# Kernel optimization log

Hardware: AMD Instinct MI355X
Metric: run time of the kernel (lower is better)

The kernel has to match this reference:

```python
import jax, jax.numpy as jnp
import numpy as np

B, L, D = 2, 4096, 2048
H, K = 32, 16              # num_heads, mini_batch_size
HD = D // H                # head_dim = 64
NMB = L // K               # 256 mini-batches
TTT_BASE_LR = 1.0
LN_EPS = 1e-6


def setup_inputs() -> dict:
    key = jax.random.key(0)
    ks = jax.random.split(key, 16)
    r = lambda k, s: 0.02 * jax.random.normal(k, s, dtype=jnp.float32)
    return {
        "hidden_states": jax.random.normal(ks[0], (B, L, D), dtype=jnp.float32),
        "wq_w": r(ks[1], (D, D)), "wq_b": r(ks[2], (D,)),
        "wk_w": r(ks[3], (D, D)), "wk_b": r(ks[4], (D,)),
        "wv_w": r(ks[5], (D, D)), "wv_b": r(ks[6], (D,)),
        "wo_w": r(ks[7], (D, D)), "wo_b": r(ks[8], (D,)),
        "ttt_norm_weight": 1.0 + r(ks[9], (H, HD)),
        "ttt_norm_bias": r(ks[10], (H, HD)),
        "lr_w": r(ks[11], (H, 1, D)),       # learnable_ttt_lr_weight
        "lr_b": r(ks[12], (H, 1)),          # learnable_ttt_lr_bias
        "W1": r(ks[13], (H, HD, HD)),
        "b1": r(ks[14], (H, 1, HD)),
        "post_norm_w": jnp.ones((D,), jnp.float32),
        "post_norm_b": jnp.zeros((D,), jnp.float32),
    }


def ln_fwd(x, gamma, beta, eps=LN_EPS):
    mu = x.mean(-1, keepdims=True)
    var = ((x - mu) ** 2).mean(-1, keepdims=True)
    return gamma * ((x - mu) / jnp.sqrt(var + eps)) + beta


def ln_fused_l2_bwd(x, l2_target, gamma, beta, eps=LN_EPS):
    # grad of 0.5*||LN(x)*gamma+beta - target||^2 w.r.t. x (standard TTT helper)
    Dd = x.shape[-1]
    mu = x.mean(-1, keepdims=True)
    var = ((x - mu) ** 2).mean(-1, keepdims=True)
    std = jnp.sqrt(var + eps)
    x_hat = (x - mu) / std
    grad_x_hat = (gamma * x_hat + beta - l2_target) * gamma
    return (Dd * grad_x_hat
            - grad_x_hat.sum(-1, keepdims=True)
            - x_hat * (x_hat * grad_x_hat).sum(-1, keepdims=True)) / (Dd * std)


def reference(hidden_states, wq_w, wq_b, wk_w, wk_b, wv_w, wv_b, wo_w, wo_b,
              ttt_norm_weight, ttt_norm_bias, lr_w, lr_b, W1, b1,
              post_norm_w, post_norm_b):
    # QKV projections
    XQ = (hidden_states @ wq_w + wq_b).reshape(B, L, H, HD)
    XK = (hidden_states @ wk_w + wk_b).reshape(B, L, H, HD)
    XV = (hidden_states @ wv_w + wv_b).reshape(B, L, H, HD)
    # L2 normalize q/k per head (F.normalize, eps=1e-12)
    XQ = XQ / jnp.maximum(jnp.linalg.norm(XQ, axis=-1, keepdims=True), 1e-12)
    XK = XK / jnp.maximum(jnp.linalg.norm(XK, axis=-1, keepdims=True), 1e-12)
    # ln_reconstruction_target: torch.std is unbiased (ddof=1), eps added to std
    diff = XV - XK
    mu = diff.mean(-1, keepdims=True)
    std = jnp.std(diff, axis=-1, ddof=1, keepdims=True)
    XV = (ttt_norm_weight[None, None] * ((diff - mu) / (std + 1e-8))
          + ttt_norm_bias[None, None]) + XK
    # reshape to mini-batches: [B,H,NMB,K,HD]
    Xmb = hidden_states.reshape(B, NMB, K, D)
    tohd = lambda t: t.transpose(0, 2, 1, 3).reshape(B, H, NMB, K, HD)
    XQ, XK, XV = tohd(XQ), tohd(XK), tohd(XV)
    # eta gate: einsum('bnkc,hdc->bhnkd') with d==1, sigmoid, scale
    ttt_lr = jnp.einsum('bnkc,hdc->bhnkd', Xmb, lr_w) + lr_b.reshape(1, H, 1, 1, 1)
    ttt_lr = jax.nn.sigmoid(ttt_lr).transpose(0, 1, 2, 4, 3) * (TTT_BASE_LR / HD)  # [B,H,NMB,1,K]
    eta = jnp.broadcast_to(ttt_lr / K, (B, H, NMB, K, K))
    ln_w = ttt_norm_weight[:, None, :]  # [H,1,HD]
    ln_b = ttt_norm_bias[:, None, :]
    tril = jnp.tril(jnp.ones((K, K), jnp.float32))
    W1s = jnp.broadcast_to(W1[None], (B, H, HD, HD))
    b1s = jnp.broadcast_to(b1[None], (B, H, 1, HD))

    def step(carry, xs):
        W1c, b1c = carry
        xq, xk, xv, eta_mb = xs  # [B,H,K,HD], eta [B,H,K,K]
        Z1 = xk @ W1c + b1c
        grad = ln_fused_l2_bwd(Z1, xv - xk, ln_w, ln_b)        # [B,H,K,HD]
        Attn1 = tril * (xq @ xk.transpose(0, 1, 3, 2))         # causal within mini-batch
        b1_bar = b1c - (tril * eta_mb) @ grad
        Z1_bar = xq @ W1c - (eta_mb * Attn1) @ grad + b1_bar
        last_eta = eta_mb[:, :, -1, :, None]                   # [B,H,K,1]
        W1n = W1c - (last_eta * xk).transpose(0, 1, 3, 2) @ grad
        b1n = b1c - jnp.sum(last_eta * grad, axis=-2, keepdims=True)
        out = xq + ln_fwd(Z1_bar, ln_w, ln_b)
        return (W1n, b1n), out

    xs = tuple(t.transpose(2, 0, 1, 3, 4) for t in (XQ, XK, XV, eta))
    _, outs = jax.lax.scan(step, (W1s, b1s), xs)               # [NMB,B,H,K,HD]
    y = outs.transpose(1, 0, 3, 2, 4).reshape(B, L, D)
    # post_norm LayerNorm(eps=1e-6) then output projection
    mu = y.mean(-1, keepdims=True)
    var = ((y - mu) ** 2).mean(-1, keepdims=True)
    y = (y - mu) / jnp.sqrt(var + 1e-6) * post_norm_w + post_norm_b
    return y @ wo_w + wo_b
```

## Files before the change

kernel.cpp:

```cpp
#include <hip/hip_runtime.h>
#include <hip/hip_bf16.h>
#include <cstdint>
#include <cstddef>

#define DEV __device__ __forceinline__

constexpr int Bb = 2, Ls = 4096, Dd = 2048, Hh = 32, HD = 64, MBK = 16, NMBc = 256;
constexpr int MTOK = Bb * Ls;

typedef __bf16 bf16x8 __attribute__((ext_vector_type(8)));
typedef float  f32x4  __attribute__((ext_vector_type(4)));

DEV unsigned short f2bf(float f) {
    union { float f; unsigned int u; } x; x.f = f;
    unsigned int u = x.u;
    return (unsigned short)((u + 0x7fffu + ((u >> 16) & 1u)) >> 16);
}
DEV float b2f(unsigned short u) {
    union { unsigned int i; float f; } x; x.i = ((unsigned int)u) << 16;
    return x.f;
}

DEV float wsum64(float v) {
    int t;
    t = __builtin_amdgcn_update_dpp(0, __float_as_int(v), 0x111, 0xf, 0xf, true); v += __int_as_float(t);
    t = __builtin_amdgcn_update_dpp(0, __float_as_int(v), 0x112, 0xf, 0xf, true); v += __int_as_float(t);
    t = __builtin_amdgcn_update_dpp(0, __float_as_int(v), 0x114, 0xf, 0xf, true); v += __int_as_float(t);
    t = __builtin_amdgcn_update_dpp(0, __float_as_int(v), 0x118, 0xf, 0xf, true); v += __int_as_float(t);
    t = __builtin_amdgcn_update_dpp(0, __float_as_int(v), 0x142, 0xa, 0xf, true); v += __int_as_float(t);
    t = __builtin_amdgcn_update_dpp(0, __float_as_int(v), 0x143, 0xc, 0xf, true); v += __int_as_float(t);
    return __int_as_float(__builtin_amdgcn_readlane(__float_as_int(v), 63));
}

DEV void g2l16(const void* g, void* l) {
    __builtin_amdgcn_global_load_lds(
        (__attribute__((address_space(1))) void*)(g),
        (__attribute__((address_space(3))) void*)(l), 16, 0, 0);
}

__global__ __launch_bounds__(256) void cast_hs_kernel(const float* __restrict__ src,
                                                      unsigned short* __restrict__ dst) {
    int i = (blockIdx.x * 256 + threadIdx.x) * 4;
    float4 v = *(const float4*)(src + i);
    ushort4 o; o.x = f2bf(v.x); o.y = f2bf(v.y); o.z = f2bf(v.z); o.w = f2bf(v.w);
    *(ushort4*)(dst + i) = o;
}

__global__ __launch_bounds__(256) void transpose_cast_kernel(const float* __restrict__ W,
                                                             unsigned short* __restrict__ Wt) {
    __shared__ float tile[64][65];
    int bx = blockIdx.x & 31;
    int by = blockIdx.x >> 5;
    int t = threadIdx.x;
    int r = t >> 4, c4 = (t & 15) * 4;
    #pragma unroll
    for (int i = 0; i < 4; ++i) {
        int row = r + i * 16;
        float4 v = *(const float4*)(W + (size_t)(bx * 64 + row) * Dd + by * 64 + c4);
        tile[row][c4 + 0] = v.x; tile[row][c4 + 1] = v.y;
        tile[row][c4 + 2] = v.z; tile[row][c4 + 3] = v.w;
    }
    __syncthreads();
    #pragma unroll
    for (int i = 0; i < 4; ++i) {
        int row = r + i * 16;
        ushort4 o;
        o.x = f2bf(tile[c4 + 0][row]); o.y = f2bf(tile[c4 + 1][row]);
        o.z = f2bf(tile[c4 + 2][row]); o.w = f2bf(tile[c4 + 3][row]);
        *(ushort4*)(Wt + (size_t)(by * 64 + row) * Dd + bx * 64 + c4) = o;
    }
}

__global__ __launch_bounds__(256) void gemm_bt_kernel(const unsigned short* __restrict__ A,
                                                      const unsigned short* __restrict__ Bt,
                                                      const float* __restrict__ bias,
                                                      float* __restrict__ C,
                                                      int M, int N, int Kd) {
    __shared__ unsigned short sA[128 * 64];
    __shared__ unsigned short sB[128 * 64];
    int t = threadIdx.x;
    int lane = t & 63;
    int wid = t >> 6, wm = wid >> 1, wn = wid & 1;
    int quad = lane >> 4, c = lane & 15;
    int bm = blockIdx.x, bn = blockIdx.y;

    const unsigned short* pa[4]; const unsigned short* pb[4];
    unsigned short* la[4]; unsigned short* lb[4];
    #pragma unroll
    for (int i = 0; i < 4; ++i) {
        int lin = i * 256 + t;
        int row = lin >> 3, blk = lin & 7;
        int oct = blk ^ (row & 7);
        pa[i] = A  + (size_t)(bm * 128 + row) * Kd + oct * 8;
        pb[i] = Bt + (size_t)(bn * 128 + row) * Kd + oct * 8;
        la[i] = sA + lin * 8;
        lb[i] = sB + lin * 8;
    }

    f32x4 acc[4][4];
    #pragma unroll
    for (int i = 0; i < 4; ++i)
        #pragma unroll
        for (int j = 0; j < 4; ++j)
            #pragma unroll
            for (int r = 0; r < 4; ++r) acc[i][j][r] = 0.f;

    const char* sAc = (const char*)sA;
    const char* sBc = (const char*)sB;
    int rowA0 = wm * 64 + c, rowB0 = wn * 64 + c;
    int sw = (c & 7);

    int nkt = Kd >> 6;
    for (int kt = 0; kt < nkt; ++kt) {
        #pragma unroll
        for (int i = 0; i < 4; ++i) {
            g2l16(pa[i], la[i]);
            g2l16(pb[i], lb[i]);
            pa[i] += 64; pb[i] += 64;
        }
        __syncthreads();
        #pragma unroll
        for (int s = 0; s < 2; ++s) {
            bf16x8 af[4], bfv[4];
            int so = (s << 2) | quad;
            #pragma unroll
            for (int mt = 0; mt < 4; ++mt)
                af[mt] = *(const bf16x8*)(sAc + (rowA0 + mt * 16) * 128 + ((so ^ sw) * 16));
            #pragma unroll
            for (int nt = 0; nt < 4; ++nt)
                bfv[nt] = *(const bf16x8*)(sBc + (rowB0 + nt * 16) * 128 + ((so ^ sw) * 16));
            #pragma unroll
            for (int mt = 0; mt < 4; ++mt)
                #pragma unroll
                for (int nt = 0; nt < 4; ++nt)
                    acc[mt][nt] = __builtin_amdgcn_mfma_f32_16x16x32_bf16(af[mt], bfv[nt], acc[mt][nt], 0, 0, 0);
        }
        __syncthreads();
    }

    float bv[4];
    #pragma unroll
    for (int nt = 0; nt < 4; ++nt) bv[nt] = bias[bn * 128 + wn * 64 + nt * 16 + c];
    #pragma unroll
    for (int mt = 0; mt < 4; ++mt)
        #pragma unroll
        for (int r = 0; r < 4; ++r) {
            int row = bm * 128 + wm * 64 + mt * 16 + quad * 4 + r;
            float* cp = C + (size_t)row * N + bn * 128 + wn * 64 + c;
            #pragma unroll
            for (int nt = 0; nt < 4; ++nt) cp[nt * 16] = acc[mt][nt][r] + bv[nt];
        }
}

__global__ __launch_bounds__(256) void fixup_kernel(float* __restrict__ XQ, float* __restrict__ XK,
                                                    float* __restrict__ XV,
                                                    const float* __restrict__ lnw_g,
                                                    const float* __restrict__ lnb_g) {
    int g = blockIdx.x * 4 + (threadIdx.x >> 6);
    int d = threadIdx.x & 63;
    int h = g & (Hh - 1);
    size_t base = (size_t)(g >> 5) * Dd + h * 64 + d;
    float q = XQ[base], k = XK[base], v = XV[base];
    float nq = sqrtf(wsum64(q * q)); q /= fmaxf(nq, 1e-12f);
    float nk = sqrtf(wsum64(k * k)); k /= fmaxf(nk, 1e-12f);
    float diff = v - k;
    float mu = wsum64(diff) * (1.f / 64.f);
    float cc = diff - mu;
    float var = wsum64(cc * cc) * (1.f / 63.f);
    float vn = lnw_g[h * 64 + d] * cc / (sqrtf(var) + 1e-8f) + lnb_g[h * 64 + d] + k;
    XQ[base] = q; XK[base] = k; XV[base] = vn;
}

__global__ __launch_bounds__(256) void lr_kernel(const float* __restrict__ hs,
                                                 const float* __restrict__ lrw,
                                                 const float* __restrict__ lrb,
                                                 float* __restrict__ lr_out) {
    int tok = blockIdx.x;
    int t = threadIdx.x;
    int h = t >> 3, j0 = t & 7;
    const float* row = hs + (size_t)tok * Dd;
    const float* wr = lrw + (size_t)h * Dd;
    float p = 0.f;
    for (int j = j0 * 4; j < Dd; j += 32) {
        float4 a = *(const float4*)(row + j);
        float4 w = *(const float4*)(wr + j);
        p += a.x * w.x + a.y * w.y + a.z * w.z + a.w * w.w;
    }
    __shared__ float red[32][8];
    red[h][j0] = p;
    __syncthreads();
    if (t < 32) {
        float s = 0.f;
        #pragma unroll
        for (int i = 0; i < 8; ++i) s += red[t][i];
        s += lrb[t];
        s = 1.f / (1.f + expf(-s));
        s *= 1.0f / (HD * MBK);
        int b = tok >> 12, l = tok & (Ls - 1);
        lr_out[(size_t)(b * Hh + t) * Ls + l] = s;
    }
}

__global__ __launch_bounds__(256, 1) void scan_kernel(const float* __restrict__ XQ,
                                                      const float* __restrict__ XK,
                                                      const float* __restrict__ XV,
                                                      const float* __restrict__ lrbuf,
                                                      const float* __restrict__ W1in,
                                                      const float* __restrict__ b1in,
                                                      const float* __restrict__ lnw_g,
                                                      const float* __restrict__ lnb_g,
                                                      float* __restrict__ Y) {
    int bh = blockIdx.x;
    int b = bh >> 5, h = bh & 31;
    int t = threadIdx.x;
    int w = t >> 6;
    int lane = t & 63;
    int q = lane >> 4, n = lane & 15;
    int gc = 16 * w + n;

    __shared__ float tiles[2][3][16 * 68];
    __shared__ float svb[2][16];
    __shared__ unsigned short wt_hi[64 * 72];
    __shared__ unsigned short wt_lo[64 * 72];
    __shared__ float zT[64 * 20];
    __shared__ float zbT[64 * 20];
    __shared__ unsigned short gbufT[64 * 32];
    __shared__ unsigned short sxkT[64 * 32];
    __shared__ float att32[16 * 32];
    __shared__ float pb[4 * 64];

    #pragma unroll
    for (int i = 0; i < 16; ++i) {
        int k = i * 4 + w;
        float val = W1in[(size_t)h * 4096 + (size_t)k * 64 + lane];
        unsigned short hi = f2bf(val);
        unsigned short lo = f2bf(val - b2f(hi));
        wt_hi[lane * 72 + k] = hi;
        wt_lo[lane * 72 + k] = lo;
    }
    #pragma unroll
    for (int i = 0; i < 8; ++i) { gbufT[i * 256 + t] = 0; sxkT[i * 256 + t] = 0; }
    #pragma unroll
    for (int i = 0; i < 2; ++i) att32[i * 256 + t] = 0.f;

    float b1r = b1in[h * 64 + lane];
    float lnwr = lnw_g[h * 64 + lane];
    float lnbr = lnb_g[h * 64 + lane];

    const size_t gbase = ((size_t)b * Ls) * Dd + h * 64;
    const float* lrp = lrbuf + (size_t)bh * Ls;

    int rowp = t >> 4, c4p = (t & 15) * 4;
    *(float4*)&tiles[0][0][rowp * 68 + c4p] = *(const float4*)(XQ + gbase + (size_t)rowp * Dd + c4p);
    *(float4*)&tiles[0][1][rowp * 68 + c4p] = *(const float4*)(XK + gbase + (size_t)rowp * Dd + c4p);
    *(float4*)&tiles[0][2][rowp * 68 + c4p] = *(const float4*)(XV + gbase + (size_t)rowp * Dd + c4p);
    if (t < 16) svb[0][t] = lrp[t];
    float4 preq = *(const float4*)(XQ + gbase + (size_t)(16 + rowp) * Dd + c4p);
    float4 prek = *(const float4*)(XK + gbase + (size_t)(16 + rowp) * Dd + c4p);
    float4 prev = *(const float4*)(XV + gbase + (size_t)(16 + rowp) * Dd + c4p);
    float presv = (t < 16) ? lrp[16 + t] : 0.f;
    __syncthreads();

    const f32x4 zero4 = {0.f, 0.f, 0.f, 0.f};

    for (int nmb = 0; nmb < NMBc; ++nmb) {
        int cb = nmb & 1, nb2 = cb ^ 1;
        int l0 = nmb * 16;
        *(float4*)&tiles[nb2][0][rowp * 68 + c4p] = preq;
        *(float4*)&tiles[nb2][1][rowp * 68 + c4p] = prek;
        *(float4*)&tiles[nb2][2][rowp * 68 + c4p] = prev;
        if (t < 16) svb[nb2][t] = presv;
        int lp = (l0 + 32 <= Ls - 16) ? (l0 + 32) : (Ls - 16);
        preq = *(const float4*)(XQ + gbase + (size_t)(lp + rowp) * Dd + c4p);
        prek = *(const float4*)(XK + gbase + (size_t)(lp + rowp) * Dd + c4p);
        prev = *(const float4*)(XV + gbase + (size_t)(lp + rowp) * Dd + c4p);
        presv = (t < 16) ? lrp[lp + t] : 0.f;

        const float* xqs = &tiles[cb][0][0];
        const float* xks = &tiles[cb][1][0];
        const float* xvs = &tiles[cb][2][0];

        bf16x8 qf0, qf1, kf0, kf1;
        {
            float4 a0 = *(const float4*)&xqs[n * 68 + 8 * q];
            float4 a1 = *(const float4*)&xqs[n * 68 + 8 * q + 4];
            float4 a2 = *(const float4*)&xqs[n * 68 + 32 + 8 * q];
            float4 a3 = *(const float4*)&xqs[n * 68 + 32 + 8 * q + 4];
            qf0[0]=(__bf16)a0.x; qf0[1]=(__bf16)a0.y; qf0[2]=(__bf16)a0.z; qf0[3]=(__bf16)a0.w;
            qf0[4]=(__bf16)a1.x; qf0[5]=(__bf16)a1.y; qf0[6]=(__bf16)a1.z; qf0[7]=(__bf16)a1.w;
            qf1[0]=(__bf16)a2.x; qf1[1]=(__bf16)a2.y; qf1[2]=(__bf16)a2.z; qf1[3]=(__bf16)a2.w;
            qf1[4]=(__bf16)a3.x; qf1[5]=(__bf16)a3.y; qf1[6]=(__bf16)a3.z; qf1[7]=(__bf16)a3.w;
            float4 k0 = *(const float4*)&xks[n * 68 + 8 * q];
            float4 k1 = *(const float4*)&xks[n * 68 + 8 * q + 4];
            float4 k2 = *(const float4*)&xks[n * 68 + 32 + 8 * q];
            float4 k3 = *(const float4*)&xks[n * 68 + 32 + 8 * q + 4];
            kf0[0]=(__bf16)k0.x; kf0[1]=(__bf16)k0.y; kf0[2]=(__bf16)k0.z; kf0[3]=(__bf16)k0.w;
            kf0[4]=(__bf16)k1.x; kf0[5]=(__bf16)k1.y; kf0[6]=(__bf16)k1.z; kf0[7]=(__bf16)k1.w;
            kf1[0]=(__bf16)k2.x; kf1[1]=(__bf16)k2.y; kf1[2]=(__bf16)k2.z; kf1[3]=(__bf16)k2.w;
            kf1[4]=(__bf16)k3.x; kf1[5]=(__bf16)k3.y; kf1[6]=(__bf16)k3.z; kf1[7]=(__bf16)k3.w;
        }
        bf16x8 wh0 = *(const bf16x8*)&wt_hi[gc * 72 + 8 * q];
        bf16x8 wh1 = *(const bf16x8*)&wt_hi[gc * 72 + 32 + 8 * q];
        bf16x8 wl0 = *(const bf16x8*)&wt_lo[gc * 72 + 8 * q];
        bf16x8 wl1 = *(const bf16x8*)&wt_lo[gc * 72 + 32 + 8 * q];

        f32x4 aacc = __builtin_amdgcn_mfma_f32_16x16x32_bf16(qf1, kf1, zero4, 0, 0, 0);
        aacc = __builtin_amdgcn_mfma_f32_16x16x32_bf16(qf0, kf0, aacc, 0, 0, 0);
        f32x4 z1 = __builtin_amdgcn_mfma_f32_16x16x32_bf16(kf0, wh0, zero4, 0, 0, 0);
        z1 = __builtin_amdgcn_mfma_f32_16x16x32_bf16(kf1, wh1, z1, 0, 0, 0);
        z1 = __builtin_amdgcn_mfma_f32_16x16x32_bf16(kf0, wl0, z1, 0, 0, 0);
        z1 = __builtin_amdgcn_mfma_f32_16x16x32_bf16(kf1, wl1, z1, 0, 0, 0);
        f32x4 zb = __builtin_amdgcn_mfma_f32_16x16x32_bf16(qf0, wh0, zero4, 0, 0, 0);
        zb = __builtin_amdgcn_mfma_f32_16x16x32_bf16(qf1, wh1, zb, 0, 0, 0);
        zb = __builtin_amdgcn_mfma_f32_16x16x32_bf16(qf0, wl0, zb, 0, 0, 0);
        zb = __builtin_amdgcn_mfma_f32_16x16x32_bf16(qf1, wl1, zb, 0, 0, 0);

        {
            float4 zs; zs.x = z1[0]; zs.y = z1[1]; zs.z = z1[2]; zs.w = z1[3];
            *(float4*)&zT[gc * 20 + 4 * q] = zs;
        }
        if (w == 0) {
            float svn = svb[cb][n];
            #pragma unroll
            for (int r = 0; r < 4; ++r) {
                int i = 4 * q + r;
                att32[i * 32 + n] = (i >= n) ? (-svn * (aacc[r] + 1.f)) : 0.f;
            }
        }
        __syncthreads();

        float4 zz = *(const float4*)&zT[lane * 20 + 4 * w];
        float zar[4] = {zz.x + b1r, zz.y + b1r, zz.z + b1r, zz.w + b1r};
        float xk_rm[4], xv_rm[4], xq_rm[4];
        #pragma unroll
        for (int r = 0; r < 4; ++r) {
            int rw = 4 * w + r;
            xk_rm[r] = xks[rw * 68 + lane];
            xv_rm[r] = xvs[rw * 68 + lane];
            xq_rm[r] = xqs[rw * 68 + lane];
        }
        float4 svr4 = *(const float4*)&svb[cb][4 * w];
        float svr[4] = {svr4.x, svr4.y, svr4.z, svr4.w};
        float gr[4]; float pbv = 0.f;
        #pragma unroll
        for (int r = 0; r < 4; ++r) {
            float s1 = wsum64(zar[r]);
            float s2 = wsum64(zar[r] * zar[r]);
            float mu = s1 * (1.f / 64.f);
            float var = s2 * (1.f / 64.f) - mu * mu;
            float rstd = rsqrtf(var + 1e-6f);
            float xh = (zar[r] - mu) * rstd;
            float g = (lnwr * xh + lnbr - (xv_rm[r] - xk_rm[r])) * lnwr;
            float sg = wsum64(g);
            float sxg = wsum64(xh * g);
            gr[r] = (64.f * g - sg - xh * sxg) * rstd * (1.f / 64.f);
            pbv += svr[r] * gr[r];
        }
        {
            ushort4 gp, sp;
            gp.x = f2bf(gr[0]); gp.y = f2bf(gr[1]); gp.z = f2bf(gr[2]); gp.w = f2bf(gr[3]);
            sp.x = f2bf(svr[0] * xk_rm[0]); sp.y = f2bf(svr[1] * xk_rm[1]);
            sp.z = f2bf(svr[2] * xk_rm[2]); sp.w = f2bf(svr[3] * xk_rm[3]);
            *(ushort4*)&gbufT[lane * 32 + 4 * w] = gp;
            *(ushort4*)&sxkT[lane * 32 + 4 * w] = sp;
            pb[w * 64 + lane] = pbv;
        }
        __syncthreads();

        bf16x8 gF = *(const bf16x8*)&gbufT[gc * 32 + 8 * q];
        bf16x8 amF;
        {
            float4 f0 = *(const float4*)&att32[n * 32 + 8 * q];
            float4 f1 = *(const float4*)&att32[n * 32 + 8 * q + 4];
            amF[0]=(__bf16)f0.x; amF[1]=(__bf16)f0.y; amF[2]=(__bf16)f0.z; amF[3]=(__bf16)f0.w;
            amF[4]=(__bf16)f1.x; amF[5]=(__bf16)f1.y; amF[6]=(__bf16)f1.z; amF[7]=(__bf16)f1.w;
        }
        zb = __builtin_amdgcn_mfma_f32_16x16x32_bf16(amF, gF, zb, 0, 0, 0);
        {
            float4 zs; zs.x = zb[0]; zs.y = zb[1]; zs.z = zb[2]; zs.w = zb[3];
            *(float4*)&zbT[gc * 20 + 4 * q] = zs;
        }
        #pragma unroll
        for (int tm = 0; tm < 4; ++tm) {
            bf16x8 ax = *(const bf16x8*)&sxkT[(16 * tm + n) * 32 + 8 * q];
            f32x4 dl = __builtin_amdgcn_mfma_f32_16x16x32_bf16(ax, gF, zero4, 0, 0, 0);
            int ko = 16 * tm + 4 * q;
            ushort4 h4 = *(ushort4*)&wt_hi[gc * 72 + ko];
            ushort4 l4 = *(ushort4*)&wt_lo[gc * 72 + ko];
            float w0 = b2f(h4.x) + b2f(l4.x) - dl[0];
            float w1 = b2f(h4.y) + b2f(l4.y) - dl[1];
            float w2 = b2f(h4.z) + b2f(l4.z) - dl[2];
            float w3 = b2f(h4.w) + b2f(l4.w) - dl[3];
            h4.x = f2bf(w0); l4.x = f2bf(w0 - b2f(h4.x));
            h4.y = f2bf(w1); l4.y = f2bf(w1 - b2f(h4.y));
            h4.z = f2bf(w2); l4.z = f2bf(w2 - b2f(h4.z));
            h4.w = f2bf(w3); l4.w = f2bf(w3 - b2f(h4.w));
            *(ushort4*)&wt_hi[gc * 72 + ko] = h4;
            *(ushort4*)&wt_lo[gc * 72 + ko] = l4;
        }
        float b1n_ = b1r - (pb[0 * 64 + lane] + pb[1 * 64 + lane] +
                            pb[2 * 64 + lane] + pb[3 * 64 + lane]);
        __syncthreads();

        float4 zz2 = *(const float4*)&zbT[lane * 20 + 4 * w];
        float zbr[4] = {zz2.x + b1r, zz2.y + b1r, zz2.z + b1r, zz2.w + b1r};
        #pragma unroll
        for (int r = 0; r < 4; ++r) {
            float s1 = wsum64(zbr[r]);
            float s2 = wsum64(zbr[r] * zbr[r]);
            float mu = s1 * (1.f / 64.f);
            float var = s2 * (1.f / 64.f) - mu * mu;
            float rstd = rsqrtf(var + 1e-6f);
            float o = lnwr * ((zbr[r] - mu) * rstd) + lnbr + xq_rm[r];
            Y[gbase + (size_t)(l0 + 4 * w + r) * Dd + lane] = o;
        }
        b1r = b1n_;
    }
}

__global__ __launch_bounds__(256) void postnorm_kernel(const float* __restrict__ Y,
                                                       const float* __restrict__ pw,
                                                       const float* __restrict__ pb,
                                                       unsigned short* __restrict__ Yb) {
    int tok = blockIdx.x, t = threadIdx.x;
    const float* row = Y + (size_t)tok * Dd;
    int c0 = t * 4, c1 = 1024 + t * 4;
    float4 v0 = *(const float4*)(row + c0);
    float4 v1 = *(const float4*)(row + c1);
    float s1 = v0.x + v0.y + v0.z + v0.w + v1.x + v1.y + v1.z + v1.w;
    float s2 = v0.x * v0.x + v0.y * v0.y + v0.z * v0.z + v0.w * v0.w +
               v1.x * v1.x + v1.y * v1.y + v1.z * v1.z + v1.w * v1.w;
    s1 = wsum64(s1); s2 = wsum64(s2);
    __shared__ float r1[4], r2[4];
    if ((t & 63) == 0) { r1[t >> 6] = s1; r2[t >> 6] = s2; }
    __syncthreads();
    float S1 = r1[0] + r1[1] + r1[2] + r1[3];
    float S2 = r2[0] + r2[1] + r2[2] + r2[3];
    float mu = S1 * (1.f / 2048.f);
    float var = S2 * (1.f / 2048.f) - mu * mu;
    float rstd = rsqrtf(var + 1e-6f);
    float4 w0 = *(const float4*)(pw + c0), b0 = *(const float4*)(pb + c0);
    float4 w1 = *(const float4*)(pw + c1), b1 = *(const float4*)(pb + c1);
    ushort4 o0, o1;
    o0.x = f2bf((v0.x - mu) * rstd * w0.x + b0.x);
    o0.y = f2bf((v0.y - mu) * rstd * w0.y + b0.y);
    o0.z = f2bf((v0.z - mu) * rstd * w0.z + b0.z);
    o0.w = f2bf((v0.w - mu) * rstd * w0.w + b0.w);
    o1.x = f2bf((v1.x - mu) * rstd * w1.x + b1.x);
    o1.y = f2bf((v1.y - mu) * rstd * w1.y + b1.y);
    o1.z = f2bf((v1.z - mu) * rstd * w1.z + b1.z);
    o1.w = f2bf((v1.w - mu) * rstd * w1.w + b1.w);
    *(ushort4*)(Yb + (size_t)tok * Dd + c0) = o0;
    *(ushort4*)(Yb + (size_t)tok * Dd + c1) = o1;
}

extern "C" void kernel_launch(void* const* d_in, const int* in_sizes, int n_in,
                              void* d_out, int out_size, void* d_ws, size_t ws_size,
                              hipStream_t stream) {
    const float* hs   = (const float*)d_in[0];
    const float* wq_w = (const float*)d_in[1];
    const float* wq_b = (const float*)d_in[2];
    const float* wk_w = (const float*)d_in[3];
    const float* wk_b = (const float*)d_in[4];
    const float* wv_w = (const float*)d_in[5];
    const float* wv_b = (const float*)d_in[6];
    const float* wo_w = (const float*)d_in[7];
    const float* wo_b = (const float*)d_in[8];
    const float* lnw  = (const float*)d_in[9];
    const float* lnb  = (const float*)d_in[10];
    const float* lr_w = (const float*)d_in[11];
    const float* lr_b = (const float*)d_in[12];
    const float* W1   = (const float*)d_in[13];
    const float* b1   = (const float*)d_in[14];
    const float* pnw  = (const float*)d_in[15];
    const float* pnb  = (const float*)d_in[16];
    float* out = (float*)d_out;

    char* ws = (char*)d_ws;
    size_t off = 0;
    auto alloc = [&](size_t bytes) -> void* {
        void* p = ws + off; off += (bytes + 255) & ~(size_t)255; return p;
    };
    unsigned short* hsb = (unsigned short*)alloc((size_t)MTOK * Dd * 2);
    unsigned short* wtb = (unsigned short*)alloc((size_t)Dd * Dd * 2);
    float* XQ = (float*)alloc((size_t)MTOK * Dd * 4);
    float* XK = (float*)alloc((size_t)MTOK * Dd * 4);
    float* XV = (float*)alloc((size_t)MTOK * Dd * 4);
    float* lrbuf = (float*)alloc((size_t)Bb * Hh * Ls * 4);
    float* Y = XQ;
    unsigned short* Yb = hsb;

    dim3 blk(256);
    cast_hs_kernel<<<dim3(MTOK * Dd / 1024), blk, 0, stream>>>(hs, hsb);

    transpose_cast_kernel<<<dim3(1024), blk, 0, stream>>>(wq_w, wtb);
    gemm_bt_kernel<<<dim3(64, 16), blk, 0, stream>>>(hsb, wtb, wq_b, XQ, MTOK, Dd, Dd);
    transpose_cast_kernel<<<dim3(1024), blk, 0, stream>>>(wk_w, wtb);
    gemm_bt_kernel<<<dim3(64, 16), blk, 0, stream>>>(hsb, wtb, wk_b, XK, MTOK, Dd, Dd);
    transpose_cast_kernel<<<dim3(1024), blk, 0, stream>>>(wv_w, wtb);
    gemm_bt_kernel<<<dim3(64, 16), blk, 0, stream>>>(hsb, wtb, wv_b, XV, MTOK, Dd, Dd);

    fixup_kernel<<<dim3(Bb * Ls * Hh / 4), blk, 0, stream>>>(XQ, XK, XV, lnw, lnb);
    lr_kernel<<<dim3(MTOK), blk, 0, stream>>>(hs, lr_w, lr_b, lrbuf);

    scan_kernel<<<dim3(Bb * Hh), blk, 0, stream>>>(XQ, XK, XV, lrbuf, W1, b1, lnw, lnb, Y);

    postnorm_kernel<<<dim3(MTOK), blk, 0, stream>>>(Y, pnw, pnb, Yb);

    transpose_cast_kernel<<<dim3(1024), blk, 0, stream>>>(wo_w, wtb);
    gemm_bt_kernel<<<dim3(64, 16), blk, 0, stream>>>(Yb, wtb, wo_b, out, MTOK, Dd, Dd);
}
```

Measured before the change: 1.566 ms.

## Fuse q/k normalization into scan staging and pre-cast bf16 operands

Removes the separate fixup kernel and performs the q/k L2 normalization and the v-target layer norm inside the scan kernel while it stages each mini-batch tile, using 16-lane DPP reductions. The staging step also writes bf16 copies of q and k, and the attention matrix is stored as bf16, so the per-step fragment conversions go away. Other changes: the hi/lo weight MFMAs now run as independent accumulation chains, the q·k MFMA moves into warp 0 only, and f2bf uses a native cast. This saves a full read and write pass over XQ/XK/XV, but adds normalization work to the serial scan's critical path.

Measured after the change: 1.413 ms. 9.8% less time.

```diff
diff --git a/kernel.cpp b/kernel.cpp
--- a/kernel.cpp
+++ b/kernel.cpp
@@ -12,9 +12,9 @@
 typedef float  f32x4  __attribute__((ext_vector_type(4)));
 
 DEV unsigned short f2bf(float f) {
-    union { float f; unsigned int u; } x; x.f = f;
-    unsigned int u = x.u;
-    return (unsigned short)((u + 0x7fffu + ((u >> 16) & 1u)) >> 16);
+    union { __bf16 h; unsigned short u; } x;
+    x.h = (__bf16)f;
+    return x.u;
 }
 DEV float b2f(unsigned short u) {
     union { unsigned int i; float f; } x; x.i = ((unsigned int)u) << 16;
@@ -30,6 +30,15 @@
     t = __builtin_amdgcn_update_dpp(0, __float_as_int(v), 0x142, 0xa, 0xf, true); v += __int_as_float(t);
     t = __builtin_amdgcn_update_dpp(0, __float_as_int(v), 0x143, 0xc, 0xf, true); v += __int_as_float(t);
     return __int_as_float(__builtin_amdgcn_readlane(__float_as_int(v), 63));
+}
+
+DEV float rsum16(float v) {
+    int t;
+    t = __builtin_amdgcn_update_dpp(0, __float_as_int(v), 0x121, 0xf, 0xf, true); v += __int_as_float(t);
+    t = __builtin_amdgcn_update_dpp(0, __float_as_int(v), 0x122, 0xf, 0xf, true); v += __int_as_float(t);
+    t = __builtin_amdgcn_update_dpp(0, __float_as_int(v), 0x124, 0xf, 0xf, true); v += __int_as_float(t);
+    t = __builtin_amdgcn_update_dpp(0, __float_as_int(v), 0x128, 0xf, 0xf, true); v += __int_as_float(t);
+    return v;
 }
 
 DEV void g2l16(const void* g, void* l) {
@@ -152,25 +161,6 @@
         }
 }
 
-__global__ __launch_bounds__(256) void fixup_kernel(float* __restrict__ XQ, float* __restrict__ XK,
-                                                    float* __restrict__ XV,
-                                                    const float* __restrict__ lnw_g,
-                                                    const float* __restrict__ lnb_g) {
-    int g = blockIdx.x * 4 + (threadIdx.x >> 6);
-    int d = threadIdx.x & 63;
-    int h = g & (Hh - 1);
-    size_t base = (size_t)(g >> 5) * Dd + h * 64 + d;
-    float q = XQ[base], k = XK[base], v = XV[base];
-    float nq = sqrtf(wsum64(q * q)); q /= fmaxf(nq, 1e-12f);
-    float nk = sqrtf(wsum64(k * k)); k /= fmaxf(nk, 1e-12f);
-    float diff = v - k;
-    float mu = wsum64(diff) * (1.f / 64.f);
-    float cc = diff - mu;
-    float var = wsum64(cc * cc) * (1.f / 63.f);
-    float vn = lnw_g[h * 64 + d] * cc / (sqrtf(var) + 1e-8f) + lnb_g[h * 64 + d] + k;
-    XQ[base] = q; XK[base] = k; XV[base] = vn;
-}
-
 __global__ __launch_bounds__(256) void lr_kernel(const float* __restrict__ hs,
                                                  const float* __restrict__ lrw,
                                                  const float* __restrict__ lrb,
@@ -199,6 +189,34 @@
         int b = tok >> 12, l = tok & (Ls - 1);
         lr_out[(size_t)(b * Hh + t) * Ls + l] = s;
     }
+}
+
+DEV void stage_qkv(float4 q, float4 k, float4 v,
+                   float* tq, float* tk, float* tv,
+                   unsigned short* bq, unsigned short* bk,
+                   int rowp, int c4p, float4 lnw4, float4 lnb4) {
+    float rq = 1.f / fmaxf(sqrtf(rsum16(q.x*q.x + q.y*q.y + q.z*q.z + q.w*q.w)), 1e-12f);
+    q.x *= rq; q.y *= rq; q.z *= rq; q.w *= rq;
+    float rk = 1.f / fmaxf(sqrtf(rsum16(k.x*k.x + k.y*k.y + k.z*k.z + k.w*k.w)), 1e-12f);
+    k.x *= rk; k.y *= rk; k.z *= rk; k.w *= rk;
+    float4 df; df.x = v.x - k.x; df.y = v.y - k.y; df.z = v.z - k.z; df.w = v.w - k.w;
+    float mu = rsum16(df.x + df.y + df.z + df.w) * (1.f / 64.f);
+    float4 cc; cc.x = df.x - mu; cc.y = df.y - mu; cc.z = df.z - mu; cc.w = df.w - mu;
+    float var = rsum16(cc.x*cc.x + cc.y*cc.y + cc.z*cc.z + cc.w*cc.w) * (1.f / 63.f);
+    float rs = 1.f / (sqrtf(var) + 1e-8f);
+    float4 vn;
+    vn.x = lnw4.x * cc.x * rs + lnb4.x + k.x;
+    vn.y = lnw4.y * cc.y * rs + lnb4.y + k.y;
+    vn.z = lnw4.z * cc.z * rs + lnb4.z + k.z;
+    vn.w = lnw4.w * cc.w * rs + lnb4.w + k.w;
+    *(float4*)&tq[rowp * 68 + c4p] = q;
+    *(float4*)&tk[rowp * 68 + c4p] = k;
+    *(float4*)&tv[rowp * 68 + c4p] = vn;
+    ushort4 qb, kb;
+    qb.x = f2bf(q.x); qb.y = f2bf(q.y); qb.z = f2bf(q.z); qb.w = f2bf(q.w);
+    kb.x = f2bf(k.x); kb.y = f2bf(k.y); kb.z = f2bf(k.z); kb.w = f2bf(k.w);
+    *(ushort4*)&bq[rowp * 72 + c4p] = qb;
+    *(ushort4*)&bk[rowp * 72 + c4p] = kb;
 }
 
 __global__ __launch_bounds__(256, 1) void scan_kernel(const float* __restrict__ XQ,
@@ -219,6 +237,8 @@
     int gc = 16 * w + n;
 
     __shared__ float tiles[2][3][16 * 68];
+    __shared__ unsigned short tbq[2][16 * 72];
+    __shared__ unsigned short tbk[2][16 * 72];
     __shared__ float svb[2][16];
     __shared__ unsigned short wt_hi[64 * 72];
     __shared__ unsigned short wt_lo[64 * 72];
@@ -226,7 +246,7 @@
     __shared__ float zbT[64 * 20];
     __shared__ unsigned short gbufT[64 * 32];
     __shared__ unsigned short sxkT[64 * 32];
-    __shared__ float att32[16 * 32];
+    __shared__ unsigned short attb[16 * 32];
     __shared__ float pb[4 * 64];
 
     #pragma unroll
@@ -241,7 +261,7 @@
     #pragma unroll
     for (int i = 0; i < 8; ++i) { gbufT[i * 256 + t] = 0; sxkT[i * 256 + t] = 0; }
     #pragma unroll
-    for (int i = 0; i < 2; ++i) att32[i * 256 + t] = 0.f;
+    for (int i = 0; i < 2; ++i) attb[i * 256 + t] = 0;
 
     float b1r = b1in[h * 64 + lane];
     float lnwr = lnw_g[h * 64 + lane];
@@ -251,9 +271,16 @@
     const float* lrp = lrbuf + (size_t)bh * Ls;
 
     int rowp = t >> 4, c4p = (t & 15) * 4;
-    *(float4*)&tiles[0][0][rowp * 68 + c4p] = *(const float4*)(XQ + gbase + (size_t)rowp * Dd + c4p);
-    *(float4*)&tiles[0][1][rowp * 68 + c4p] = *(const float4*)(XK + gbase + (size_t)rowp * Dd + c4p);
-    *(float4*)&tiles[0][2][rowp * 68 + c4p] = *(const float4*)(XV + gbase + (size_t)rowp * Dd + c4p);
+    float4 lnw4 = *(const float4*)(lnw_g + h * 64 + c4p);
+    float4 lnb4 = *(const float4*)(lnb_g + h * 64 + c4p);
+
+    {
+        float4 q0 = *(const float4*)(XQ + gbase + (size_t)rowp * Dd + c4p);
+        float4 k0 = *(const float4*)(XK + gbase + (size_t)rowp * Dd + c4p);
+        float4 v0 = *(const float4*)(XV + gbase + (size_t)rowp * Dd + c4p);
+        stage_qkv(q0, k0, v0, &tiles[0][0][0], &tiles[0][1][0], &tiles[0][2][0],
+                  tbq[0], tbk[0], rowp, c4p, lnw4, lnb4);
+    }
     if (t < 16) svb[0][t] = lrp[t];
     float4 preq = *(const float4*)(XQ + gbase + (size_t)(16 + rowp) * Dd + c4p);
     float4 prek = *(const float4*)(XK + gbase + (size_t)(16 + rowp) * Dd + c4p);
@@ -266,9 +293,8 @@
     for (int nmb = 0; nmb < NMBc; ++nmb) {
         int cb = nmb & 1, nb2 = cb ^ 1;
         int l0 = nmb * 16;
-        *(float4*)&tiles[nb2][0][rowp * 68 + c4p] = preq;
-        *(float4*)&tiles[nb2][1][rowp * 68 + c4p] = prek;
-        *(float4*)&tiles[nb2][2][rowp * 68 + c4p] = prev;
+        stage_qkv(preq, prek, prev, &tiles[nb2][0][0], &tiles[nb2][1][0], &tiles[nb2][2][0],
+                  tbq[nb2], tbk[nb2], rowp, c4p, lnw4, lnb4);
         if (t < 16) svb[nb2][t] = presv;
         int lp = (l0 + 32 <= Ls - 16) ? (l0 + 32) : (Ls - 16);
         preq = *(const float4*)(XQ + gbase + (size_t)(lp + rowp) * Dd + c4p);
@@ -279,52 +305,42 @@
         const float* xqs = &tiles[cb][0][0];
         const float* xks = &tiles[cb][1][0];
         const float* xvs = &tiles[cb][2][0];
-
-        bf16x8 qf0, qf1, kf0, kf1;
-        {
-            float4 a0 = *(const float4*)&xqs[n * 68 + 8 * q];
-            float4 a1 = *(const float4*)&xqs[n * 68 + 8 * q + 4];
-            float4 a2 = *(const float4*)&xqs[n * 68 + 32 + 8 * q];
-            float4 a3 = *(const float4*)&xqs[n * 68 + 32 + 8 * q + 4];
-            qf0[0]=(__bf16)a0.x; qf0[1]=(__bf16)a0.y; qf0[2]=(__bf16)a0.z; qf0[3]=(__bf16)a0.w;
-            qf0[4]=(__bf16)a1.x; qf0[5]=(__bf16)a1.y; qf0[6]=(__bf16)a1.z; qf0[7]=(__bf16)a1.w;
-            qf1[0]=(__bf16)a2.x; qf1[1]=(__bf16)a2.y; qf1[2]=(__bf16)a2.z; qf1[3]=(__bf16)a2.w;
-            qf1[4]=(__bf16)a3.x; qf1[5]=(__bf16)a3.y; qf1[6]=(__bf16)a3.z; qf1[7]=(__bf16)a3.w;
-            float4 k0 = *(const float4*)&xks[n * 68 + 8 * q];
-            float4 k1 = *(const float4*)&xks[n * 68 + 8 * q + 4];
-            float4 k2 = *(const float4*)&xks[n * 68 + 32 + 8 * q];
-            float4 k3 = *(const float4*)&xks[n * 68 + 32 + 8 * q + 4];
-            kf0[0]=(__bf16)k0.x; kf0[1]=(__bf16)k0.y; kf0[2]=(__bf16)k0.z; kf0[3]=(__bf16)k0.w;
-            kf0[4]=(__bf16)k1.x; kf0[5]=(__bf16)k1.y; kf0[6]=(__bf16)k1.z; kf0[7]=(__bf16)k1.w;
-            kf1[0]=(__bf16)k2.x; kf1[1]=(__bf16)k2.y; kf1[2]=(__bf16)k2.z; kf1[3]=(__bf16)k2.w;
-            kf1[4]=(__bf16)k3.x; kf1[5]=(__bf16)k3.y; kf1[6]=(__bf16)k3.z; kf1[7]=(__bf16)k3.w;
-        }
+        const unsigned short* bqs = tbq[cb];
+        const unsigned short* bks = tbk[cb];
+
+        bf16x8 qf0 = *(const bf16x8*)&bqs[n * 72 + 8 * q];
+        bf16x8 qf1 = *(const bf16x8*)&bqs[n * 72 + 32 + 8 * q];
+        bf16x8 kf0 = *(const bf16x8*)&bks[n * 72 + 8 * q];
+        bf16x8 kf1 = *(const bf16x8*)&bks[n * 72 + 32 + 8 * q];
+
         bf16x8 wh0 = *(const bf16x8*)&wt_hi[gc * 72 + 8 * q];
         bf16x8 wh1 = *(const bf16x8*)&wt_hi[gc * 72 + 32 + 8 * q];
         bf16x8 wl0 = *(const bf16x8*)&wt_lo[gc * 72 + 8 * q];
         bf16x8 wl1 = *(const bf16x8*)&wt_lo[gc * 72 + 32 + 8 * q];
 
-        f32x4 aacc = __builtin_amdgcn_mfma_f32_16x16x32_bf16(qf1, kf1, zero4, 0, 0, 0);
-        aacc = __builtin_amdgcn_mfma_f32_16x16x32_bf16(qf0, kf0, aacc, 0, 0, 0);
         f32x4 z1 = __builtin_amdgcn_mfma_f32_16x16x32_bf16(kf0, wh0, zero4, 0, 0, 0);
         z1 = __builtin_amdgcn_mfma_f32_16x16x32_bf16(kf1, wh1, z1, 0, 0, 0);
-        z1 = __builtin_amdgcn_mfma_f32_16x16x32_bf16(kf0, wl0, z1, 0, 0, 0);
-        z1 = __builtin_amdgcn_mfma_f32_16x16x32_bf16(kf1, wl1, z1, 0, 0, 0);
+        f32x4 z1l = __builtin_amdgcn_mfma_f32_16x16x32_bf16(kf0, wl0, zero4, 0, 0, 0);
+        z1l = __builtin_amdgcn_mfma_f32_16x16x32_bf16(kf1, wl1, z1l, 0, 0, 0);
+        z1 = z1 + z1l;
         f32x4 zb = __builtin_amdgcn_mfma_f32_16x16x32_bf16(qf0, wh0, zero4, 0, 0, 0);
         zb = __builtin_amdgcn_mfma_f32_16x16x32_bf16(qf1, wh1, zb, 0, 0, 0);
-        zb = __builtin_amdgcn_mfma_f32_16x16x32_bf16(qf0, wl0, zb, 0, 0, 0);
-        zb = __builtin_amdgcn_mfma_f32_16x16x32_bf16(qf1, wl1, zb, 0, 0, 0);
+        f32x4 zbl = __builtin_amdgcn_mfma_f32_16x16x32_bf16(qf0, wl0, zero4, 0, 0, 0);
+        zbl = __builtin_amdgcn_mfma_f32_16x16x32_bf16(qf1, wl1, zbl, 0, 0, 0);
+        zb = zb + zbl;
 
         {
             float4 zs; zs.x = z1[0]; zs.y = z1[1]; zs.z = z1[2]; zs.w = z1[3];
             *(float4*)&zT[gc * 20 + 4 * q] = zs;
         }
         if (w == 0) {
+            f32x4 aacc = __builtin_amdgcn_mfma_f32_16x16x32_bf16(qf1, kf1, zero4, 0, 0, 0);
+            aacc = __builtin_amdgcn_mfma_f32_16x16x32_bf16(qf0, kf0, aacc, 0, 0, 0);
             float svn = svb[cb][n];
             #pragma unroll
             for (int r = 0; r < 4; ++r) {
                 int i = 4 * q + r;
-                att32[i * 32 + n] = (i >= n) ? (-svn * (aacc[r] + 1.f)) : 0.f;
+                attb[i * 32 + n] = f2bf((i >= n) ? (-svn * (aacc[r] + 1.f)) : 0.f);
             }
         }
         __syncthreads();
@@ -368,13 +384,7 @@
         __syncthreads();
 
         bf16x8 gF = *(const bf16x8*)&gbufT[gc * 32 + 8 * q];
-        bf16x8 amF;
-        {
-            float4 f0 = *(const float4*)&att32[n * 32 + 8 * q];
-            float4 f1 = *(const float4*)&att32[n * 32 + 8 * q + 4];
-            amF[0]=(__bf16)f0.x; amF[1]=(__bf16)f0.y; amF[2]=(__bf16)f0.z; amF[3]=(__bf16)f0.w;
-            amF[4]=(__bf16)f1.x; amF[5]=(__bf16)f1.y; amF[6]=(__bf16)f1.z; amF[7]=(__bf16)f1.w;
-        }
+        bf16x8 amF = *(const bf16x8*)&attb[n * 32 + 8 * q];
         zb = __builtin_amdgcn_mfma_f32_16x16x32_bf16(amF, gF, zb, 0, 0, 0);
         {
             float4 zs; zs.x = zb[0]; zs.y = zb[1]; zs.z = zb[2]; zs.w = zb[3];
@@ -500,7 +510,6 @@
     transpose_cast_kernel<<<dim3(1024), blk, 0, stream>>>(wv_w, wtb);
     gemm_bt_kernel<<<dim3(64, 16), blk, 0, stream>>>(hsb, wtb, wv_b, XV, MTOK, Dd, Dd);
 
-    fixup_kernel<<<dim3(Bb * Ls * Hh / 4), blk, 0, stream>>>(XQ, XK, XV, lnw, lnb);
     lr_kernel<<<dim3(MTOK), blk, 0, stream>>>(hs, lr_w, lr_b, lrbuf);
 
     scan_kernel<<<dim3(Bb * Hh), blk, 0, stream>>>(XQ, XK, XV, lrbuf, W1, b1, lnw, lnb, Y);
```
